# Optimization experiments

Measured on AMD Instinct MI355X. Metric: run time of the kernel, lower is better.

The kernel has to match this reference:

```python
import jax, jax.numpy as jnp
from jax import lax
import numpy as np

INPUT_SIZE = 256
HIDDEN = 256


def _gru_scan(x, W_ih, W_hh, b_ih, b_hh):
    # x: [b, t, in], PyTorch GRU gate order: r, z, n
    b, t, _ = x.shape
    k = W_hh.shape[1]
    # precompute input contribution for all timesteps: [b, t, 3k]
    gx = jnp.einsum('bti,gi->btg', x, W_ih) + b_ih

    def step(h, gxt):
        gh = h @ W_hh.T + b_hh                 # [b, 3k]
        xr, xz, xn = jnp.split(gxt, 3, axis=-1)
        hr, hz, hn = jnp.split(gh, 3, axis=-1)
        r = jax.nn.sigmoid(xr + hr)
        z = jax.nn.sigmoid(xz + hz)
        n = jnp.tanh(xn + r * hn)
        h_new = (1.0 - z) * n + z * h
        return h_new, h_new

    h0 = jnp.zeros((b, k), x.dtype)
    _, hs = lax.scan(step, h0, jnp.swapaxes(gx, 0, 1))  # hs: [t, b, k]
    return hs


def setup_inputs() -> dict:
    key = jax.random.key(0)
    kx, k1, k2, k3, k4 = jax.random.split(key, 5)
    s_ih = 1.0 / np.sqrt(HIDDEN)
    x = jax.random.normal(kx, (32, 2048, INPUT_SIZE), dtype=jnp.float32)
    W_ih = jax.random.uniform(k1, (3 * HIDDEN, INPUT_SIZE), jnp.float32, -s_ih, s_ih)
    W_hh = jax.random.uniform(k2, (3 * HIDDEN, HIDDEN), jnp.float32, -s_ih, s_ih)
    b_ih = jax.random.uniform(k3, (3 * HIDDEN,), jnp.float32, -s_ih, s_ih)
    b_hh = jax.random.uniform(k4, (3 * HIDDEN,), jnp.float32, -s_ih, s_ih)
    return {'x': x, 'W_ih': W_ih, 'W_hh': W_hh, 'b_ih': b_ih, 'b_hh': b_hh}


def reference(x, W_ih, W_hh, b_ih, b_hh):
    # forward direction
    hs_f = _gru_scan(x, W_ih, W_hh, b_ih, b_hh)                     # [t, b, k]
    # 'bidirectional': same weights applied to time-reversed input
    hs_r = _gru_scan(x[:, ::-1, :], W_ih, W_hh, b_ih, b_hh)[::-1]   # [t, b, k]
    outputs = jnp.concatenate(
        (jnp.swapaxes(hs_f, 0, 1), jnp.swapaxes(hs_r, 0, 1)), axis=2)  # [b, t, 2k]
    hiddens = jnp.concatenate((hs_f, hs_r), axis=2)                    # [t, b, 2k]
    return outputs, hiddens
```

## Files before the change

kernel.cpp:

```cpp
#include <hip/hip_runtime.h>
#include <hip/hip_fp16.h>


typedef __fp16 half2_t __attribute__((ext_vector_type(2)));

static constexpr int T_STEPS = 2048;
static constexpr int BATCH   = 32;
static constexpr int HID     = 256;
static constexpr int IN      = 256;
static constexpr int G3      = 768;

__device__ __forceinline__ float fdot2(half2_t a, half2_t b, float c) {
    return __builtin_amdgcn_fdot2(a, b, c, false);
}

__device__ __forceinline__ void barrier_lgkm() {
    asm volatile("s_waitcnt lgkmcnt(0)\n\ts_barrier" ::: "memory");
}

__global__ __launch_bounds__(256, 2) void gx_gemm(
        const float* __restrict__ x,
        const float* __restrict__ Wih,
        const float* __restrict__ bih,
        _Float16* __restrict__ gx) {
    __shared__ ushort As[64 * 256];
    __shared__ ushort Bs[64 * 256];

    const int tid = threadIdx.x;
    const int m0  = blockIdx.x * 64;
    const int tx  = tid & 15;
    const int ty  = tid >> 4;

#pragma unroll
    for (int i = 0; i < 16; ++i) {
        int f    = tid + 256 * i;
        int row  = f >> 6;
        int col4 = f & 63;
        float4 v = *(const float4*)(x + (size_t)(m0 + row) * IN + col4 * 4);
        half2_t h0 = __builtin_amdgcn_cvt_pkrtz(v.x, v.y);
        half2_t h1 = __builtin_amdgcn_cvt_pkrtz(v.z, v.w);
        int chunk = col4 >> 1;
        int idx = row * 256 + ((chunk ^ (row & 7)) * 8) + (col4 & 1) * 4;
        uint2 wv;
        wv.x = __builtin_bit_cast(unsigned, h0);
        wv.y = __builtin_bit_cast(unsigned, h1);
        *(uint2*)(As + idx) = wv;
    }

    for (int nb = 0; nb < 12; ++nb) {
#pragma unroll
        for (int i = 0; i < 16; ++i) {
            int f    = tid + 256 * i;
            int row  = f >> 6;
            int col4 = f & 63;
            float4 v = *(const float4*)(Wih + (size_t)(nb * 64 + row) * IN + col4 * 4);
            half2_t h0 = __builtin_amdgcn_cvt_pkrtz(v.x, v.y);
            half2_t h1 = __builtin_amdgcn_cvt_pkrtz(v.z, v.w);
            int chunk = col4 >> 1;
            int idx = row * 256 + ((chunk ^ (row & 7)) * 8) + (col4 & 1) * 4;
            uint2 wv;
            wv.x = __builtin_bit_cast(unsigned, h0);
            wv.y = __builtin_bit_cast(unsigned, h1);
            *(uint2*)(Bs + idx) = wv;
        }
        barrier_lgkm();

        float acc[4][4];
#pragma unroll
        for (int jm = 0; jm < 4; ++jm)
#pragma unroll
            for (int jn = 0; jn < 4; ++jn) acc[jm][jn] = 0.f;

#pragma unroll 4
        for (int kc = 0; kc < 32; ++kc) {
            union { uint4 u; half2_t h[4]; } av[4], bv[4];
#pragma unroll
            for (int jm = 0; jm < 4; ++jm) {
                int r = ty * 4 + jm;
                av[jm].u = *(const uint4*)(As + r * 256 + ((kc ^ (r & 7)) * 8));
            }
#pragma unroll
            for (int jn = 0; jn < 4; ++jn) {
                int r = tx + 16 * jn;
                bv[jn].u = *(const uint4*)(Bs + r * 256 + ((kc ^ (r & 7)) * 8));
            }
#pragma unroll
            for (int jm = 0; jm < 4; ++jm)
#pragma unroll
                for (int jn = 0; jn < 4; ++jn)
#pragma unroll
                    for (int p = 0; p < 4; ++p)
                        acc[jm][jn] = fdot2(av[jm].h[p], bv[jn].h[p], acc[jm][jn]);
        }

#pragma unroll
        for (int jn = 0; jn < 4; ++jn) {
            int n = nb * 64 + tx + 16 * jn;
            float bias = bih[n];
#pragma unroll
            for (int jm = 0; jm < 4; ++jm) {
                int m = m0 + ty * 4 + jm;
                gx[(size_t)m * G3 + n] = (_Float16)(acc[jm][jn] + bias);
            }
        }
        barrier_lgkm();
    }
}

__attribute__((amdgpu_waves_per_eu(3, 3)))
__global__ __launch_bounds__(768) void gru_seq(
        const _Float16* __restrict__ gx,
        const float* __restrict__ Whh,
        const float* __restrict__ bhh,
        float* __restrict__ out0,
        float* __restrict__ out1) {
    __shared__ float  P[4 * 768];
    __shared__ ushort h16[256];
    __shared__ ushort gxb[768];

    const int tid = threadIdx.x;
    const int b   = blockIdx.x & 31;
    const int d   = blockIdx.x >> 5;
    const int w   = tid >> 6;
    const int L   = tid & 63;
    const int s   = w & 3;
    const int g   = w >> 2;

    half2_t Wr[4][32];
    float   Wb[4];
#pragma unroll
    for (int jr = 0; jr < 4; ++jr) {
        const int row = g * 256 + jr * 64 + L;
        const float* wrow = Whh + (size_t)row * HID + s * 64;
#pragma unroll
        for (int q = 0; q < 32; ++q) {
            float2 wv = *(const float2*)(wrow + 2 * q);
            Wr[jr][q] = __builtin_amdgcn_cvt_pkrtz(wv.x, wv.y);
        }
        Wb[jr] = (s == 0) ? bhh[row] : 0.f;
    }

    float hprev = 0.f;
    if (tid < 256) h16[tid] = 0;

    const int tp0 = d ? (T_STEPS - 1) : 0;
    const int sgn = d ? -1 : 1;

    const _Float16* gp = gx + ((size_t)b * T_STEPS + tp0) * G3 + tid * 8;
    const int gpd = sgn * G3;
    uint4 greg{};
    if (tid < 96) greg = *(const uint4*)gp;

    float* o0 = out0 + ((size_t)b * T_STEPS + tp0) * 512 + d * 256 + tid;
    float* o1 = out1 + ((size_t)tp0 * BATCH + b) * 512 + d * 256 + tid;
    const int o0d = sgn * 512;
    const int o1d = sgn * (BATCH * 512);

    __syncthreads();

    for (int t = 0; t < T_STEPS; ++t) {
        if (tid < 96) {
            *(uint4*)(gxb + tid * 8) = greg;
            if (t + 1 < T_STEPS) {
                gp += gpd;
                greg = *(const uint4*)gp;
            }
        }

        float acc[4] = {Wb[0], Wb[1], Wb[2], Wb[3]};
#pragma unroll
        for (int c = 0; c < 4; ++c) {
            union { uint4 u; half2_t h[4]; } hh0, hh1;
            hh0.u = *(const uint4*)(h16 + s * 64 + c * 16);
            hh1.u = *(const uint4*)(h16 + s * 64 + c * 16 + 8);
#pragma unroll
            for (int jr = 0; jr < 4; ++jr) {
#pragma unroll
                for (int p = 0; p < 4; ++p) {
                    acc[jr] = fdot2(Wr[jr][c * 8 + p],     hh0.h[p], acc[jr]);
                    acc[jr] = fdot2(Wr[jr][c * 8 + 4 + p], hh1.h[p], acc[jr]);
                }
            }
        }
#pragma unroll
        for (int jr = 0; jr < 4; ++jr)
            P[s * 768 + g * 256 + jr * 64 + L] = acc[jr];

        barrier_lgkm();

        if (tid < 256) {
            const int i = tid;
            float hr = (P[i]       + P[768 + i])  + (P[1536 + i] + P[2304 + i]);
            float hz = (P[256 + i] + P[1024 + i]) + (P[1792 + i] + P[2560 + i]);
            float hn = (P[512 + i] + P[1280 + i]) + (P[2048 + i] + P[2816 + i]);
            const _Float16* gxh = (const _Float16*)gxb;
            float xr = (float)gxh[i]       + hr;
            float xz = (float)gxh[256 + i] + hz;
            float r = __builtin_amdgcn_rcpf(1.f + __builtin_amdgcn_exp2f(xr * -1.44269504f));
            float z = __builtin_amdgcn_rcpf(1.f + __builtin_amdgcn_exp2f(xz * -1.44269504f));
            float nx = (float)gxh[512 + i] + r * hn;
            float e2 = __builtin_amdgcn_exp2f(nx * 2.88539008f);
            float n  = 1.f - 2.f * __builtin_amdgcn_rcpf(1.f + e2);
            float h  = n + z * (hprev - n);
            hprev = h;

            h16[i] = __builtin_bit_cast(ushort, (_Float16)h);
            *o0 = h; *o1 = h;
            o0 += o0d; o1 += o1d;
        }
        barrier_lgkm();
    }
}

extern "C" void kernel_launch(void* const* d_in, const int* in_sizes, int n_in,
                              void* d_out, int out_size, void* d_ws, size_t ws_size,
                              hipStream_t stream) {
    const float* x   = (const float*)d_in[0];
    const float* Wih = (const float*)d_in[1];
    const float* Whh = (const float*)d_in[2];
    const float* bih = (const float*)d_in[3];
    const float* bhh = (const float*)d_in[4];

    float* out0 = (float*)d_out;
    float* out1 = out0 + (size_t)BATCH * T_STEPS * 512;

    _Float16* gx = (_Float16*)d_ws;

    gx_gemm<<<dim3(65536 / 64), dim3(256), 0, stream>>>(x, Wih, bih, gx);
    gru_seq<<<dim3(BATCH * 2), dim3(768), 0, stream>>>(gx, Whh, bhh, out0, out1);
}
```

Before: 2.553 ms.

## Use MFMA for recurrent matvec and fold r/z hidden biases into gx

Replaces the per-lane fdot2 recurrent mat-vec in the sequential GRU kernel with 16x16x32 f16 MFMA instructions. Weights are held in MFMA A-fragment layout, and the h vector is broadcast as the B operand, so only one column of each MFMA output is useful and lane 0 of each 16-lane group writes the partials. The r and z parts of b_hh are folded into the gx GEMM bias, while the n-gate hidden bias stays in the elementwise stage. The gx prefetch moves to waves 8-9 and the waves_per_eu attribute is removed. This trades wasted MFMA lanes for fewer VALU instructions on the latency-critical serial step.

```diff
diff --git a/kernel.cpp b/kernel.cpp
--- a/kernel.cpp
+++ b/kernel.cpp
@@ -3,6 +3,8 @@
 
 
 typedef __fp16 half2_t __attribute__((ext_vector_type(2)));
+typedef __fp16 half8_t __attribute__((ext_vector_type(8)));
+typedef float  f32x4   __attribute__((ext_vector_type(4)));
 
 static constexpr int T_STEPS = 2048;
 static constexpr int BATCH   = 32;
@@ -22,6 +24,7 @@
         const float* __restrict__ x,
         const float* __restrict__ Wih,
         const float* __restrict__ bih,
+        const float* __restrict__ bhh,
         _Float16* __restrict__ gx) {
     __shared__ ushort As[64 * 256];
     __shared__ ushort Bs[64 * 256];
@@ -96,7 +99,7 @@
 #pragma unroll
         for (int jn = 0; jn < 4; ++jn) {
             int n = nb * 64 + tx + 16 * jn;
-            float bias = bih[n];
+            float bias = bih[n] + (n < 512 ? bhh[n] : 0.f);
 #pragma unroll
             for (int jm = 0; jm < 4; ++jm) {
                 int m = m0 + ty * 4 + jm;
@@ -107,7 +110,6 @@
     }
 }
 
-__attribute__((amdgpu_waves_per_eu(3, 3)))
 __global__ __launch_bounds__(768) void gru_seq(
         const _Float16* __restrict__ gx,
         const float* __restrict__ Whh,
@@ -121,70 +123,88 @@
     const int tid = threadIdx.x;
     const int b   = blockIdx.x & 31;
     const int d   = blockIdx.x >> 5;
-    const int w   = tid >> 6;
     const int L   = tid & 63;
-    const int s   = w & 3;
-    const int g   = w >> 2;
-
-    half2_t Wr[4][32];
-    float   Wb[4];
-#pragma unroll
-    for (int jr = 0; jr < 4; ++jr) {
-        const int row = g * 256 + jr * 64 + L;
-        const float* wrow = Whh + (size_t)row * HID + s * 64;
-#pragma unroll
-        for (int q = 0; q < 32; ++q) {
-            float2 wv = *(const float2*)(wrow + 2 * q);
-            Wr[jr][q] = __builtin_amdgcn_cvt_pkrtz(wv.x, wv.y);
-        }
-        Wb[jr] = (s == 0) ? bhh[row] : 0.f;
-    }
-
-    float hprev = 0.f;
-    if (tid < 256) h16[tid] = 0;
+    const int s   = (tid >> 6) & 3;
+    const int g   = tid >> 8;
+
+    half8_t Wf[32];
+    {
+        const int mrow = L & 15;
+        const int klo  = (L >> 4) * 8;
+#pragma unroll
+        for (int mt = 0; mt < 16; ++mt)
+#pragma unroll
+            for (int kh = 0; kh < 2; ++kh) {
+                const float* p = Whh + (size_t)(g * 256 + mt * 16 + mrow) * HID
+                               + s * 64 + kh * 32 + klo;
+                union { half8_t v; half2_t h[4]; } u;
+#pragma unroll
+                for (int q = 0; q < 4; ++q) {
+                    float2 f = *(const float2*)(p + 2 * q);
+                    u.h[q] = __builtin_amdgcn_cvt_pkrtz(f.x, f.y);
+                }
+                Wf[mt * 2 + kh] = u.v;
+            }
+    }
+
+    float hprev = 0.f, bh_n = 0.f;
+    if (tid < 256) {
+        bh_n = bhh[512 + tid];
+        h16[tid] = 0;
+    }
 
     const int tp0 = d ? (T_STEPS - 1) : 0;
     const int sgn = d ? -1 : 1;
 
-    const _Float16* gp = gx + ((size_t)b * T_STEPS + tp0) * G3 + tid * 8;
+    const int pt = tid - 512;
+    const bool pf = (unsigned)pt < 96u;
+    const _Float16* gp = gx + ((size_t)b * T_STEPS + tp0) * G3 + (pf ? pt * 8 : 0);
     const int gpd = sgn * G3;
     uint4 greg{};
-    if (tid < 96) greg = *(const uint4*)gp;
+    if (pf) greg = *(const uint4*)gp;
 
     float* o0 = out0 + ((size_t)b * T_STEPS + tp0) * 512 + d * 256 + tid;
     float* o1 = out1 + ((size_t)tp0 * BATCH + b) * 512 + d * 256 + tid;
     const int o0d = sgn * 512;
     const int o1d = sgn * (BATCH * 512);
 
+    const ushort* hseg = h16 + s * 64 + (L >> 4) * 8;
+    float* pw = P + s * 768 + g * 256 + (L >> 4) * 4;
+    const bool wr = (L & 15) == 0;
+
     __syncthreads();
 
     for (int t = 0; t < T_STEPS; ++t) {
-        if (tid < 96) {
-            *(uint4*)(gxb + tid * 8) = greg;
+        if (pf) {
+            *(uint4*)(gxb + pt * 8) = greg;
             if (t + 1 < T_STEPS) {
                 gp += gpd;
                 greg = *(const uint4*)gp;
             }
         }
 
-        float acc[4] = {Wb[0], Wb[1], Wb[2], Wb[3]};
-#pragma unroll
-        for (int c = 0; c < 4; ++c) {
-            union { uint4 u; half2_t h[4]; } hh0, hh1;
-            hh0.u = *(const uint4*)(h16 + s * 64 + c * 16);
-            hh1.u = *(const uint4*)(h16 + s * 64 + c * 16 + 8);
-#pragma unroll
-            for (int jr = 0; jr < 4; ++jr) {
-#pragma unroll
-                for (int p = 0; p < 4; ++p) {
-                    acc[jr] = fdot2(Wr[jr][c * 8 + p],     hh0.h[p], acc[jr]);
-                    acc[jr] = fdot2(Wr[jr][c * 8 + 4 + p], hh1.h[p], acc[jr]);
-                }
-            }
-        }
-#pragma unroll
-        for (int jr = 0; jr < 4; ++jr)
-            P[s * 768 + g * 256 + jr * 64 + L] = acc[jr];
+        union { uint4 u; half8_t v; } b0, b1;
+        b0.u = *(const uint4*)hseg;
+        b1.u = *(const uint4*)(hseg + 32);
+
+#pragma unroll
+        for (int grp = 0; grp < 4; ++grp) {
+            f32x4 z = {0.f, 0.f, 0.f, 0.f};
+            f32x4 a0 = __builtin_amdgcn_mfma_f32_16x16x32_f16(Wf[8*grp+0], b0.v, z, 0, 0, 0);
+            f32x4 a1 = __builtin_amdgcn_mfma_f32_16x16x32_f16(Wf[8*grp+2], b0.v, z, 0, 0, 0);
+            f32x4 a2 = __builtin_amdgcn_mfma_f32_16x16x32_f16(Wf[8*grp+4], b0.v, z, 0, 0, 0);
+            f32x4 a3 = __builtin_amdgcn_mfma_f32_16x16x32_f16(Wf[8*grp+6], b0.v, z, 0, 0, 0);
+            a0 = __builtin_amdgcn_mfma_f32_16x16x32_f16(Wf[8*grp+1], b1.v, a0, 0, 0, 0);
+            a1 = __builtin_amdgcn_mfma_f32_16x16x32_f16(Wf[8*grp+3], b1.v, a1, 0, 0, 0);
+            a2 = __builtin_amdgcn_mfma_f32_16x16x32_f16(Wf[8*grp+5], b1.v, a2, 0, 0, 0);
+            a3 = __builtin_amdgcn_mfma_f32_16x16x32_f16(Wf[8*grp+7], b1.v, a3, 0, 0, 0);
+            if (wr) {
+                *(f32x4*)(pw + (grp * 4 + 0) * 16) = a0;
+                *(f32x4*)(pw + (grp * 4 + 1) * 16) = a1;
+                *(f32x4*)(pw + (grp * 4 + 2) * 16) = a2;
+                *(f32x4*)(pw + (grp * 4 + 3) * 16) = a3;
+            }
+        }
 
         barrier_lgkm();
 
@@ -198,7 +218,7 @@
             float xz = (float)gxh[256 + i] + hz;
             float r = __builtin_amdgcn_rcpf(1.f + __builtin_amdgcn_exp2f(xr * -1.44269504f));
             float z = __builtin_amdgcn_rcpf(1.f + __builtin_amdgcn_exp2f(xz * -1.44269504f));
-            float nx = (float)gxh[512 + i] + r * hn;
+            float nx = (float)gxh[512 + i] + r * (hn + bh_n);
             float e2 = __builtin_amdgcn_exp2f(nx * 2.88539008f);
             float n  = 1.f - 2.f * __builtin_amdgcn_rcpf(1.f + e2);
             float h  = n + z * (hprev - n);
@@ -226,6 +246,6 @@
 
     _Float16* gx = (_Float16*)d_ws;
 
-    gx_gemm<<<dim3(65536 / 64), dim3(256), 0, stream>>>(x, Wih, bih, gx);
+    gx_gemm<<<dim3(65536 / 64), dim3(256), 0, stream>>>(x, Wih, bih, bhh, gx);
     gru_seq<<<dim3(BATCH * 2), dim3(768), 0, stream>>>(gx, Whh, bhh, out0, out1);
 }
```

Measured after the change: 4.158 ms. 62.8% more time.
